# Optimization experiments

Measured on AMD Instinct MI355X. Metric: run time of the kernel, lower is better.

The kernel has to match this reference:

```python
import jax, jax.numpy as jnp
import numpy as np

# static config (matches init_kwargs)
T_K = 3      # Time_kernel
K = 3        # spatial_kernel_side_length
C = 64       # dim_hidden
H = 4        # num_head
D = 16       # dim_head
NL = 2       # num_layers
F = 3        # dim_feature
N, S1, S2 = 32, 32, 32
P = K // 2
L1 = T_K // 2
M = T_K * K * K
EPS = 1e-5


def _neighbor_mask():
    # spatial_neighbor_mask with an all-ones city mask: offset (k1,k2) is a valid
    # neighbor of cell (s1,s2) iff it lands inside the grid.
    m = np.zeros((S1, S2, K, K), dtype=bool)
    s1 = np.arange(S1); s2 = np.arange(S2)
    for k1 in range(K):
        v1 = (s1 + k1 - P >= 0) & (s1 + k1 - P < S1)
        for k2 in range(K):
            v2 = (s2 + k2 - P >= 0) & (s2 + k2 - P < S2)
            m[:, :, k1, k2] = v1[:, None] & v2[None, :]
    mf = m.reshape(S1, S2, K * K)
    # tiled across Time_kernel, flattened in (t, k1, k2) order like the torch code
    return np.tile(mf[:, :, None, :], (1, 1, T_K, 1)).reshape(S1, S2, M)

_MASK = jnp.asarray(_neighbor_mask())


def _forward(x, W_in, b_in, W_out, b_out, Wq, bq, Wk, bk, Wv, bv):
    # BatchNorm2d (training-mode batch stats, affine = identity init)
    mean = x.mean(axis=(0, 1, 2))
    var = ((x - mean) ** 2).mean(axis=(0, 1, 2))
    h = (x - mean) * jax.lax.rsqrt(var + EPS)
    h = h @ W_in + b_in  # [N,S1,S2,C]

    for l in range(NL):
        res = h  # res_block_thickness = 1 -> residual every layer
        q = (h @ Wq[l] + bq[l]).reshape(N, S1, S2, H, D)
        # spatial unfold (nn.Unfold, padding=K//2, stride=1)
        hp = jnp.pad(h, ((0, 0), (P, P), (P, P), (0, 0)))
        u = jnp.stack([jnp.stack([hp[:, k1:k1 + S1, k2:k2 + S2, :]
                                  for k2 in range(K)]) for k1 in range(K)])  # [K,K,N,S1,S2,C]
        # time unfold (zero-padded shifts along N)
        up = jnp.pad(u, ((0, 0), (0, 0), (L1, L1), (0, 0), (0, 0), (0, 0)))
        ut = jnp.stack([up[:, :, t:t + N] for t in range(T_K)])  # [T,K,K,N,S1,S2,C]
        # per-offset single-Linear MLPs (kernel_neurons=[C,C]), batched over T,K,K
        ks = jnp.einsum('tijnabc,tijcd->nabtijd', ut, Wk[l]) + bk[l]
        vs = jnp.einsum('tijnabc,tijcd->nabtijd', ut, Wv[l]) + bv[l]
        kM = ks.reshape(N, S1, S2, M, H, D)
        vM = vs.reshape(N, S1, S2, M, H, D)
        # unscaled dot-product attention over valid neighbors (masked == dropped)
        sc = jnp.einsum('nabmhd,nabhd->nabhm', kM, q)
        sc = jnp.where(_MASK[None, :, :, None, :], sc, -1e30)
        w = jax.nn.softmax(sc, axis=-1)
        h = jnp.einsum('nabhm,nabmhd->nabhd', w, vM).reshape(N, S1, S2, C)
        h = h + res

    return h @ W_out + b_out  # [N,S1,S2,F]


def setup_inputs() -> dict:
    key = jax.random.key(0)
    k = jax.random.split(key, 11)
    s = 0.05
    return {
        'x': jax.random.normal(k[0], (N, S1, S2, F), jnp.float32),
        'W_in': jax.random.normal(k[1], (F, C), jnp.float32) * s,
        'b_in': jax.random.normal(k[2], (C,), jnp.float32) * s,
        'W_out': jax.random.normal(k[3], (C, F), jnp.float32) * s,
        'b_out': jax.random.normal(k[4], (F,), jnp.float32) * s,
        'Wq': jax.random.normal(k[5], (NL, C, C), jnp.float32) * s,
        'bq': jax.random.normal(k[6], (NL, C), jnp.float32) * s,
        'Wk': jax.random.normal(k[7], (NL, T_K, K, K, C, C), jnp.float32) * s,
        'bk': jax.random.normal(k[8], (NL, T_K, K, K, C), jnp.float32) * s,
        'Wv': jax.random.normal(k[9], (NL, T_K, K, K, C, C), jnp.float32) * s,
        'bv': jax.random.normal(k[10], (NL, T_K, K, K, C), jnp.float32) * s,
    }


def reference(x, W_in, b_in, W_out, b_out, Wq, bq, Wk, bk, Wv, bv):
    return _forward(x, W_in, b_in, W_out, b_out, Wq, bq, Wk, bk, Wv, bv)
```

## Files before the change

kernel.cpp:

```cpp
#include <hip/hip_runtime.h>
#include <hip/hip_bf16.h>


typedef short short8_t __attribute__((ext_vector_type(8)));
typedef float floatx4 __attribute__((ext_vector_type(4)));

__device__ __forceinline__ short f2bs(float f) {
    __hip_bfloat16 h = __float2bfloat16(f);
    return *reinterpret_cast<short*>(&h);
}
__device__ __forceinline__ float bs2f(short s) {
    union { unsigned u; float f; } v;
    v.u = ((unsigned)(unsigned short)s) << 16;
    return v.f;
}
__device__ __forceinline__ int hn_idx(int rowid, int chunk) {
    return rowid * 64 + ((chunk ^ (rowid & 7)) << 3);
}

__global__ void prep_kernel(const float* __restrict__ Wq, const float* __restrict__ Wk,
                            const float* __restrict__ Wv, short* __restrict__ dst,
                            const float* __restrict__ x, float* __restrict__ sums) {
    if (blockIdx.x < 220) {
        int t = blockIdx.x * 256 + threadIdx.x;
        if (t >= 110 * 512) return;
        int mat  = t >> 9;
        int rem  = t & 511;
        int kk   = rem >> 8;
        int nt   = (rem >> 6) & 3;
        int lane = rem & 63;
        int krow = kk * 32 + (lane >> 4) * 8;
        int col  = nt * 16 + (lane & 15);
        const float* W;
        if (mat < 2)       W = Wq + mat * 4096;
        else if (mat < 56) W = Wk + (mat - 2) * 4096;
        else               W = Wv + (mat - 56) * 4096;
        short8_t v;
        #pragma unroll
        for (int j = 0; j < 8; ++j) v[j] = f2bs(W[(krow + j) * 64 + col]);
        *(short8_t*)&dst[(size_t)mat * 4096 + ((kk * 4 + nt) * 64 + lane) * 8] = v;
    } else {
        int bid = blockIdx.x - 220;
        int t = bid * 256 + threadIdx.x;
        const float4* x4 = (const float4*)x;
        float4 v0 = x4[t * 3 + 0], v1 = x4[t * 3 + 1], v2 = x4[t * 3 + 2];
        float vv[6];
        vv[0] = v0.x + v0.w + v1.z + v2.y;
        vv[1] = v0.y + v1.x + v1.w + v2.z;
        vv[2] = v0.z + v1.y + v2.x + v2.w;
        vv[3] = v0.x*v0.x + v0.w*v0.w + v1.z*v1.z + v2.y*v2.y;
        vv[4] = v0.y*v0.y + v1.x*v1.x + v1.w*v1.w + v2.z*v2.z;
        vv[5] = v0.z*v0.z + v1.y*v1.y + v2.x*v2.x + v2.w*v2.w;
        #pragma unroll
        for (int i = 0; i < 6; ++i) {
            #pragma unroll
            for (int off = 1; off < 64; off <<= 1) vv[i] += __shfl_xor(vv[i], off);
        }
        __shared__ float part[4][6];
        if ((threadIdx.x & 63) == 0) {
            #pragma unroll
            for (int i = 0; i < 6; ++i) part[threadIdx.x >> 6][i] = vv[i];
        }
        __syncthreads();
        if (threadIdx.x < 6)
            sums[bid * 8 + threadIdx.x] = part[0][threadIdx.x] + part[1][threadIdx.x] +
                                          part[2][threadIdx.x] + part[3][threadIdx.x];
    }
}

template <bool FIRST>
__global__ __launch_bounds__(512, 4)
void layer_fused(const float* __restrict__ x, const float* __restrict__ sums,
                 const float* __restrict__ W_in, const float* __restrict__ b_in,
                 const short* __restrict__ hbf_in, short* __restrict__ hbf_out,
                 const float* __restrict__ Wout, const float* __restrict__ bout,
                 float* __restrict__ out,
                 const short* __restrict__ wqB, const float* __restrict__ bq,
                 const short* __restrict__ wkB, const float* __restrict__ bk,
                 const short* __restrict__ wvB, const float* __restrict__ bv) {
    __shared__ short HnS[324 * 64];
    __shared__ float Waux[256];
    __shared__ float bn6[6];

    const int tid = threadIdx.x;
    const int bb0 = blockIdx.x * 4, a = blockIdx.y, nb = blockIdx.z;

    if (FIRST) {
        if (tid < 3) {
            float s = 0.f, qq = 0.f;
            #pragma unroll
            for (int p = 0; p < 32; ++p) { s += sums[p * 8 + tid]; qq += sums[p * 8 + 3 + tid]; }
            float mean = s * (1.f / 32768.f);
            float var  = qq * (1.f / 32768.f) - mean * mean;
            bn6[tid]     = mean;
            bn6[3 + tid] = rsqrtf(var + 1e-5f);
        }
        if (tid < 192)      Waux[tid] = W_in[tid];
        else if (tid < 256) Waux[tid] = b_in[tid - 192];
    } else {
        if (tid < 192)      Waux[tid] = Wout[tid];
        else if (tid < 195) Waux[tid] = bout[tid - 192];
    }
    __syncthreads();

    float mean0 = 0, mean1 = 0, mean2 = 0, rs0 = 0, rs1 = 0, rs2 = 0;
    if (FIRST) {
        mean0 = bn6[0]; mean1 = bn6[1]; mean2 = bn6[2];
        rs0 = bn6[3]; rs1 = bn6[4]; rs2 = bn6[5];
    }

    for (int id = tid; id < 2592; id += 512) {
        int rowid = id >> 3, cc = id & 7;
        int r = rowid % 18;
        int rw = rowid / 18;
        int spa = rw / 6, jcol = rw - spa * 6;
        int aa = a + spa - 1, bb = bb0 + jcol - 1;
        int n  = nb * 16 + r - 1;
        short8_t v = {0, 0, 0, 0, 0, 0, 0, 0};
        if ((unsigned)n < 32u && (unsigned)aa < 32u && (unsigned)bb < 32u) {
            int cell = (n * 32 + aa) * 32 + bb;
            if (FIRST) {
                float xn0 = (x[cell*3+0] - mean0) * rs0;
                float xn1 = (x[cell*3+1] - mean1) * rs1;
                float xn2 = (x[cell*3+2] - mean2) * rs2;
                #pragma unroll
                for (int j = 0; j < 8; ++j) {
                    int c = cc * 8 + j;
                    float h = Waux[192+c] + xn0*Waux[c] + xn1*Waux[64+c] + xn2*Waux[128+c];
                    v[j] = f2bs(h);
                }
            } else {
                v = *(const short8_t*)&hbf_in[cell * 64 + cc * 8];
            }
        }
        *(short8_t*)&HnS[hn_idx(rowid, cc)] = v;
    }
    __syncthreads();

    const int lane = tid & 63;
    const int wv8  = tid >> 6;
    const int w    = wv8 & 3;
    const int g2   = wv8 >> 2;
    const int e    = lane & 15;
    const int q    = lane >> 4;
    const int c0   = w * 16 + q * 4;

    bool va[3], vb[6];
    #pragma unroll
    for (int d = 0; d < 3; ++d) va[d] = (unsigned)(a + d - 1) < 32u;
    #pragma unroll
    for (int j = 0; j < 6; ++j) vb[j] = (unsigned)(bb0 + j - 1) < 32u;

    floatx4 qv[4];
    {
        short8_t wq0 = *(const short8_t*)&wqB[((0 * 4 + w) * 64 + lane) * 8];
        short8_t wq1 = *(const short8_t*)&wqB[((1 * 4 + w) * 64 + lane) * 8];
        const float4 bq4 = *(const float4*)&bq[c0];
        #pragma unroll
        for (int ci = 0; ci < 4; ++ci) {
            const int row = (6 + ci + 1) * 18 + e + 1;
            short8_t h0 = *(const short8_t*)&HnS[hn_idx(row, q)];
            short8_t h1 = *(const short8_t*)&HnS[hn_idx(row, 4 + q)];
            floatx4 acc = {0, 0, 0, 0};
            acc = __builtin_amdgcn_mfma_f32_16x16x32_bf16(wq0, h0, acc, 0, 0, 0);
            acc = __builtin_amdgcn_mfma_f32_16x16x32_bf16(wq1, h1, acc, 0, 0, 0);
            qv[ci][0] = acc[0] + bq4.x; qv[ci][1] = acc[1] + bq4.y;
            qv[ci][2] = acc[2] + bq4.z; qv[ci][3] = acc[3] + bq4.w;
        }
    }

    floatx4 o[4] = {{0,0,0,0},{0,0,0,0},{0,0,0,0},{0,0,0,0}};
    float ss[4] = {0.f, 0.f, 0.f, 0.f};

    const int mstart = g2 ? 14 : 0;
    const int mend   = g2 ? 27 : 14;
    for (int m = mstart; m < mend; ++m) {
        const int t  = (m * 57) >> 9;
        const int sp = m - 9 * t;
        const int di = (sp * 11) >> 5;
        const int dj = sp - 3 * di;
        if (!va[di]) continue;
        short8_t wk0 = *(const short8_t*)&wkB[m * 4096 + ((0 * 4 + w) * 64 + lane) * 8];
        short8_t wk1 = *(const short8_t*)&wkB[m * 4096 + ((1 * 4 + w) * 64 + lane) * 8];
        short8_t wv0 = *(const short8_t*)&wvB[m * 4096 + ((0 * 4 + w) * 64 + lane) * 8];
        short8_t wv1 = *(const short8_t*)&wvB[m * 4096 + ((1 * 4 + w) * 64 + lane) * 8];
        const float4 bk4 = *(const float4*)&bk[m * 64 + c0];
        const float4 bv4 = *(const float4*)&bv[m * 64 + c0];
        const int rowb = (di * 6 + dj) * 18 + e + t;
        #pragma unroll
        for (int ci = 0; ci < 4; ++ci) {
            if (!vb[dj + ci]) continue;
            const int row = rowb + ci * 18;
            short8_t h0 = *(const short8_t*)&HnS[hn_idx(row, q)];
            short8_t h1 = *(const short8_t*)&HnS[hn_idx(row, 4 + q)];
            floatx4 kacc = {0, 0, 0, 0};
            kacc = __builtin_amdgcn_mfma_f32_16x16x32_bf16(wk0, h0, kacc, 0, 0, 0);
            kacc = __builtin_amdgcn_mfma_f32_16x16x32_bf16(wk1, h1, kacc, 0, 0, 0);
            floatx4 vacc = {0, 0, 0, 0};
            vacc = __builtin_amdgcn_mfma_f32_16x16x32_bf16(wv0, h0, vacc, 0, 0, 0);
            vacc = __builtin_amdgcn_mfma_f32_16x16x32_bf16(wv1, h1, vacc, 0, 0, 0);
            float p = (kacc[0] + bk4.x) * qv[ci][0] + (kacc[1] + bk4.y) * qv[ci][1]
                    + (kacc[2] + bk4.z) * qv[ci][2] + (kacc[3] + bk4.w) * qv[ci][3];
            p += __shfl_xor(p, 16);
            p += __shfl_xor(p, 32);
            float wgt = __expf(p);
            ss[ci] += wgt;
            o[ci][0] += wgt * (vacc[0] + bv4.x);
            o[ci][1] += wgt * (vacc[1] + bv4.y);
            o[ci][2] += wgt * (vacc[2] + bv4.z);
            o[ci][3] += wgt * (vacc[3] + bv4.w);
        }
    }

    __syncthreads();
    float* stbuf = (float*)HnS;
    if (g2 == 1) {
        #pragma unroll
        for (int ci = 0; ci < 4; ++ci) {
            float* d = &stbuf[(((w * 64 + lane) * 4) + ci) * 5];
            d[0] = ss[ci];
            d[1] = o[ci][0]; d[2] = o[ci][1]; d[3] = o[ci][2]; d[4] = o[ci][3];
        }
    }
    __syncthreads();
    if (g2 == 0) {
        #pragma unroll
        for (int ci = 0; ci < 4; ++ci) {
            const float* d = &stbuf[(((w * 64 + lane) * 4) + ci) * 5];
            float inv = 1.0f / (ss[ci] + d[0]);
            o[ci][0] = (o[ci][0] + d[1]) * inv;
            o[ci][1] = (o[ci][1] + d[2]) * inv;
            o[ci][2] = (o[ci][2] + d[3]) * inv;
            o[ci][3] = (o[ci][3] + d[4]) * inv;
        }
    }

    const int n = nb * 16 + e;
    if (FIRST) {
        if (g2 == 0) {
            #pragma unroll
            for (int ci = 0; ci < 4; ++ci) {
                int cell = (n * 32 + a) * 32 + bb0 + ci;
                float xn0 = (x[cell*3+0] - mean0) * rs0;
                float xn1 = (x[cell*3+1] - mean1) * rs1;
                float xn2 = (x[cell*3+2] - mean2) * rs2;
                short4 hb; short* hbp = (short*)&hb;
                #pragma unroll
                for (int i = 0; i < 4; ++i) {
                    int c = c0 + i;
                    float res = Waux[192+c] + xn0*Waux[c] + xn1*Waux[64+c] + xn2*Waux[128+c];
                    hbp[i] = f2bs(o[ci][i] + res);
                }
                *(short4*)&hbf_out[cell * 64 + c0] = hb;
            }
        }
    } else {
        __syncthreads();
        float* hf = (float*)HnS;
        if (g2 == 0) {
            #pragma unroll
            for (int ci = 0; ci < 4; ++ci) {
                int cell = (n * 32 + a) * 32 + bb0 + ci;
                short4 hb = *(const short4*)&hbf_in[cell * 64 + c0];
                float* d = &hf[(ci * 16 + e) * 68 + c0];
                d[0] = o[ci][0] + bs2f(hb.x);
                d[1] = o[ci][1] + bs2f(hb.y);
                d[2] = o[ci][2] + bs2f(hb.z);
                d[3] = o[ci][3] + bs2f(hb.w);
            }
        }
        __syncthreads();
        if (tid < 192) {
            int rowglob = tid / 3, f = tid - rowglob * 3;
            int ci = rowglob >> 4, row = rowglob & 15;
            float acc = Waux[192 + f];
            #pragma unroll 8
            for (int cc = 0; cc < 64; ++cc) acc += hf[rowglob * 68 + cc] * Waux[cc * 3 + f];
            int nn = nb * 16 + row;
            out[((nn * 32 + a) * 32 + bb0 + ci) * 3 + f] = acc;
        }
    }
}

extern "C" void kernel_launch(void* const* d_in, const int* in_sizes, int n_in,
                              void* d_out, int out_size, void* d_ws, size_t ws_size,
                              hipStream_t stream) {
    const float* x     = (const float*)d_in[0];
    const float* W_in  = (const float*)d_in[1];
    const float* b_in  = (const float*)d_in[2];
    const float* W_out = (const float*)d_in[3];
    const float* b_out = (const float*)d_in[4];
    const float* Wq    = (const float*)d_in[5];
    const float* bq    = (const float*)d_in[6];
    const float* Wk    = (const float*)d_in[7];
    const float* bk    = (const float*)d_in[8];
    const float* Wv    = (const float*)d_in[9];
    const float* bv    = (const float*)d_in[10];

    float* ws    = (float*)d_ws;
    float* sums  = ws;
    short* h1bf  = (short*)(ws + 256);
    short* wB    = h1bf + 2097152;
    float* out   = (float*)d_out;

    prep_kernel<<<252, 256, 0, stream>>>(Wq, Wk, Wv, wB, x, sums);

    const short* wq0 = wB;                const short* wq1 = wB + 4096;
    const short* wk0 = wB + 2 * 4096;     const short* wk1 = wB + (2 + 27) * 4096;
    const short* wv0 = wB + 56 * 4096;    const short* wv1 = wB + (56 + 27) * 4096;

    dim3 grid(8, 32, 2);
    layer_fused<true><<<grid, 512, 0, stream>>>(
        x, sums, W_in, b_in, nullptr, h1bf, nullptr, nullptr, nullptr,
        wq0, bq, wk0, bk, wv0, bv);
    layer_fused<false><<<grid, 512, 0, stream>>>(
        nullptr, nullptr, nullptr, nullptr, h1bf, nullptr, W_out, b_out, out,
        wq1, bq + 64, wk1, bk + 1728, wv1, bv + 1728);
}
```

Baseline: 144.9 us.

## Switch attention projections to 32x32x16 MFMA with all-32-batch tiles

Replaces the 16x16x32 bf16 MFMA tiles with 32x32x16 tiles. Each block now covers all 32 batch (time) rows for 2 columns instead of 16 rows for 4 columns, and the weight repack in the prep kernel is changed to match the new fragment layout. Each wave computes half the channels (32) for one cell column, so two heads' logits reduce with a single cross-lane shuffle. This is meant to raise MFMA efficiency and cut duplicated shared-memory halo loads along the time axis. In exchange it uses a larger LDS tile and more accumulator registers, which may lower occupancy, and the grid becomes 16x32.

```diff
diff --git a/kernel.cpp b/kernel.cpp
--- a/kernel.cpp
+++ b/kernel.cpp
@@ -3,7 +3,7 @@
 
 
 typedef short short8_t __attribute__((ext_vector_type(8)));
-typedef float floatx4 __attribute__((ext_vector_type(4)));
+typedef float floatx16 __attribute__((ext_vector_type(16)));
 
 __device__ __forceinline__ short f2bs(float f) {
     __hip_bfloat16 h = __float2bfloat16(f);
@@ -16,6 +16,18 @@
 }
 __device__ __forceinline__ int hn_idx(int rowid, int chunk) {
     return rowid * 64 + ((chunk ^ (rowid & 7)) << 3);
+}
+__device__ __forceinline__ floatx16 bias_frag(const float* __restrict__ p) {
+    float4 f0 = *(const float4*)(p);
+    float4 f1 = *(const float4*)(p + 8);
+    float4 f2 = *(const float4*)(p + 16);
+    float4 f3 = *(const float4*)(p + 24);
+    floatx16 c;
+    c[0]=f0.x;  c[1]=f0.y;  c[2]=f0.z;  c[3]=f0.w;
+    c[4]=f1.x;  c[5]=f1.y;  c[6]=f1.z;  c[7]=f1.w;
+    c[8]=f2.x;  c[9]=f2.y;  c[10]=f2.z; c[11]=f2.w;
+    c[12]=f3.x; c[13]=f3.y; c[14]=f3.z; c[15]=f3.w;
+    return c;
 }
 
 __global__ void prep_kernel(const float* __restrict__ Wq, const float* __restrict__ Wk,
@@ -26,11 +38,11 @@
         if (t >= 110 * 512) return;
         int mat  = t >> 9;
         int rem  = t & 511;
-        int kk   = rem >> 8;
-        int nt   = (rem >> 6) & 3;
+        int kk   = rem >> 7;
+        int ch   = (rem >> 6) & 1;
         int lane = rem & 63;
-        int krow = kk * 32 + (lane >> 4) * 8;
-        int col  = nt * 16 + (lane & 15);
+        int krow = kk * 16 + (lane >> 5) * 8;
+        int col  = ch * 32 + (lane & 31);
         const float* W;
         if (mat < 2)       W = Wq + mat * 4096;
         else if (mat < 56) W = Wk + (mat - 2) * 4096;
@@ -38,7 +50,7 @@
         short8_t v;
         #pragma unroll
         for (int j = 0; j < 8; ++j) v[j] = f2bs(W[(krow + j) * 64 + col]);
-        *(short8_t*)&dst[(size_t)mat * 4096 + ((kk * 4 + nt) * 64 + lane) * 8] = v;
+        *(short8_t*)&dst[(size_t)mat * 4096 + ((kk * 2 + ch) * 64 + lane) * 8] = v;
     } else {
         int bid = blockIdx.x - 220;
         int t = bid * 256 + threadIdx.x;
@@ -78,12 +90,13 @@
                  const short* __restrict__ wqB, const float* __restrict__ bq,
                  const short* __restrict__ wkB, const float* __restrict__ bk,
                  const short* __restrict__ wvB, const float* __restrict__ bv) {
-    __shared__ short HnS[324 * 64];
+    __shared__ short HnS[408 * 64];
     __shared__ float Waux[256];
     __shared__ float bn6[6];
 
     const int tid = threadIdx.x;
-    const int bb0 = blockIdx.x * 4, a = blockIdx.y, nb = blockIdx.z;
+    const int b0  = blockIdx.x * 2;
+    const int a   = blockIdx.y;
 
     if (FIRST) {
         if (tid < 3) {
@@ -109,13 +122,13 @@
         rs0 = bn6[3]; rs1 = bn6[4]; rs2 = bn6[5];
     }
 
-    for (int id = tid; id < 2592; id += 512) {
+    for (int id = tid; id < 3264; id += 512) {
         int rowid = id >> 3, cc = id & 7;
-        int r = rowid % 18;
-        int rw = rowid / 18;
-        int spa = rw / 6, jcol = rw - spa * 6;
-        int aa = a + spa - 1, bb = bb0 + jcol - 1;
-        int n  = nb * 16 + r - 1;
+        int rw = (rowid * 241) >> 13;
+        int r  = rowid - rw * 34;
+        int spa = rw >> 2, jc = rw & 3;
+        int aa = a + spa - 1, bb = b0 + jc - 1;
+        int n  = r - 1;
         short8_t v = {0, 0, 0, 0, 0, 0, 0, 0};
         if ((unsigned)n < 32u && (unsigned)aa < 32u && (unsigned)bb < 32u) {
             int cell = (n * 32 + aa) * 32 + bb;
@@ -139,38 +152,35 @@
 
     const int lane = tid & 63;
     const int wv8  = tid >> 6;
-    const int w    = wv8 & 3;
+    const int cw   = wv8 & 1;
+    const int ch   = (wv8 >> 1) & 1;
     const int g2   = wv8 >> 2;
-    const int e    = lane & 15;
-    const int q    = lane >> 4;
-    const int c0   = w * 16 + q * 4;
-
-    bool va[3], vb[6];
+    const int nn   = lane & 31;
+    const int h5   = lane >> 5;
+    const int cb4  = ch * 32 + 4 * h5;
+
+    bool va[3], vvb[3];
     #pragma unroll
-    for (int d = 0; d < 3; ++d) va[d] = (unsigned)(a + d - 1) < 32u;
+    for (int d = 0; d < 3; ++d) {
+        va[d]  = (unsigned)(a + d - 1) < 32u;
+        vvb[d] = (unsigned)(b0 + cw + d - 1) < 32u;
+    }
+
+    floatx16 qc = bias_frag(bq + cb4);
+    {
+        const int rq = (4 + cw + 1) * 34 + nn + 1;
+        #pragma unroll
+        for (int kk = 0; kk < 4; ++kk) {
+            short8_t wf = *(const short8_t*)&wqB[((kk * 2 + ch) * 64 + lane) * 8];
+            short8_t bf = *(const short8_t*)&HnS[hn_idx(rq, kk * 2 + h5)];
+            qc = __builtin_amdgcn_mfma_f32_32x32x16_bf16(wf, bf, qc, 0, 0, 0);
+        }
+    }
+
+    floatx16 o;
     #pragma unroll
-    for (int j = 0; j < 6; ++j) vb[j] = (unsigned)(bb0 + j - 1) < 32u;
-
-    floatx4 qv[4];
-    {
-        short8_t wq0 = *(const short8_t*)&wqB[((0 * 4 + w) * 64 + lane) * 8];
-        short8_t wq1 = *(const short8_t*)&wqB[((1 * 4 + w) * 64 + lane) * 8];
-        const float4 bq4 = *(const float4*)&bq[c0];
-        #pragma unroll
-        for (int ci = 0; ci < 4; ++ci) {
-            const int row = (6 + ci + 1) * 18 + e + 1;
-            short8_t h0 = *(const short8_t*)&HnS[hn_idx(row, q)];
-            short8_t h1 = *(const short8_t*)&HnS[hn_idx(row, 4 + q)];
-            floatx4 acc = {0, 0, 0, 0};
-            acc = __builtin_amdgcn_mfma_f32_16x16x32_bf16(wq0, h0, acc, 0, 0, 0);
-            acc = __builtin_amdgcn_mfma_f32_16x16x32_bf16(wq1, h1, acc, 0, 0, 0);
-            qv[ci][0] = acc[0] + bq4.x; qv[ci][1] = acc[1] + bq4.y;
-            qv[ci][2] = acc[2] + bq4.z; qv[ci][3] = acc[3] + bq4.w;
-        }
-    }
-
-    floatx4 o[4] = {{0,0,0,0},{0,0,0,0},{0,0,0,0},{0,0,0,0}};
-    float ss[4] = {0.f, 0.f, 0.f, 0.f};
+    for (int r = 0; r < 16; ++r) o[r] = 0.f;
+    float ss0 = 0.f, ss1 = 0.f;
 
     const int mstart = g2 ? 14 : 0;
     const int mend   = g2 ? 27 : 14;
@@ -179,105 +189,109 @@
         const int sp = m - 9 * t;
         const int di = (sp * 11) >> 5;
         const int dj = sp - 3 * di;
-        if (!va[di]) continue;
-        short8_t wk0 = *(const short8_t*)&wkB[m * 4096 + ((0 * 4 + w) * 64 + lane) * 8];
-        short8_t wk1 = *(const short8_t*)&wkB[m * 4096 + ((1 * 4 + w) * 64 + lane) * 8];
-        short8_t wv0 = *(const short8_t*)&wvB[m * 4096 + ((0 * 4 + w) * 64 + lane) * 8];
-        short8_t wv1 = *(const short8_t*)&wvB[m * 4096 + ((1 * 4 + w) * 64 + lane) * 8];
-        const float4 bk4 = *(const float4*)&bk[m * 64 + c0];
-        const float4 bv4 = *(const float4*)&bv[m * 64 + c0];
-        const int rowb = (di * 6 + dj) * 18 + e + t;
-        #pragma unroll
-        for (int ci = 0; ci < 4; ++ci) {
-            if (!vb[dj + ci]) continue;
-            const int row = rowb + ci * 18;
-            short8_t h0 = *(const short8_t*)&HnS[hn_idx(row, q)];
-            short8_t h1 = *(const short8_t*)&HnS[hn_idx(row, 4 + q)];
-            floatx4 kacc = {0, 0, 0, 0};
-            kacc = __builtin_amdgcn_mfma_f32_16x16x32_bf16(wk0, h0, kacc, 0, 0, 0);
-            kacc = __builtin_amdgcn_mfma_f32_16x16x32_bf16(wk1, h1, kacc, 0, 0, 0);
-            floatx4 vacc = {0, 0, 0, 0};
-            vacc = __builtin_amdgcn_mfma_f32_16x16x32_bf16(wv0, h0, vacc, 0, 0, 0);
-            vacc = __builtin_amdgcn_mfma_f32_16x16x32_bf16(wv1, h1, vacc, 0, 0, 0);
-            float p = (kacc[0] + bk4.x) * qv[ci][0] + (kacc[1] + bk4.y) * qv[ci][1]
-                    + (kacc[2] + bk4.z) * qv[ci][2] + (kacc[3] + bk4.w) * qv[ci][3];
-            p += __shfl_xor(p, 16);
-            p += __shfl_xor(p, 32);
-            float wgt = __expf(p);
-            ss[ci] += wgt;
-            o[ci][0] += wgt * (vacc[0] + bv4.x);
-            o[ci][1] += wgt * (vacc[1] + bv4.y);
-            o[ci][2] += wgt * (vacc[2] + bv4.z);
-            o[ci][3] += wgt * (vacc[3] + bv4.w);
-        }
+        if (!va[di] || !vvb[dj]) continue;
+        const int rowb = (di * 4 + cw + dj) * 34 + nn + t;
+        short8_t bfr0 = *(const short8_t*)&HnS[hn_idx(rowb, 0 * 2 + h5)];
+        short8_t bfr1 = *(const short8_t*)&HnS[hn_idx(rowb, 1 * 2 + h5)];
+        short8_t bfr2 = *(const short8_t*)&HnS[hn_idx(rowb, 2 * 2 + h5)];
+        short8_t bfr3 = *(const short8_t*)&HnS[hn_idx(rowb, 3 * 2 + h5)];
+        const short* wkp = wkB + m * 4096 + (ch * 64 + lane) * 8;
+        const short* wvp = wvB + m * 4096 + (ch * 64 + lane) * 8;
+        floatx16 kc = bias_frag(bk + m * 64 + cb4);
+        kc = __builtin_amdgcn_mfma_f32_32x32x16_bf16(*(const short8_t*)(wkp),        bfr0, kc, 0, 0, 0);
+        kc = __builtin_amdgcn_mfma_f32_32x32x16_bf16(*(const short8_t*)(wkp + 1024), bfr1, kc, 0, 0, 0);
+        kc = __builtin_amdgcn_mfma_f32_32x32x16_bf16(*(const short8_t*)(wkp + 2048), bfr2, kc, 0, 0, 0);
+        kc = __builtin_amdgcn_mfma_f32_32x32x16_bf16(*(const short8_t*)(wkp + 3072), bfr3, kc, 0, 0, 0);
+        floatx16 vc = bias_frag(bv + m * 64 + cb4);
+        vc = __builtin_amdgcn_mfma_f32_32x32x16_bf16(*(const short8_t*)(wvp),        bfr0, vc, 0, 0, 0);
+        vc = __builtin_amdgcn_mfma_f32_32x32x16_bf16(*(const short8_t*)(wvp + 1024), bfr1, vc, 0, 0, 0);
+        vc = __builtin_amdgcn_mfma_f32_32x32x16_bf16(*(const short8_t*)(wvp + 2048), bfr2, vc, 0, 0, 0);
+        vc = __builtin_amdgcn_mfma_f32_32x32x16_bf16(*(const short8_t*)(wvp + 3072), bfr3, vc, 0, 0, 0);
+        float p0 = 0.f, p1 = 0.f;
+        #pragma unroll
+        for (int r = 0; r < 8; ++r)  p0 += kc[r] * qc[r];
+        #pragma unroll
+        for (int r = 8; r < 16; ++r) p1 += kc[r] * qc[r];
+        p0 += __shfl_xor(p0, 32);
+        p1 += __shfl_xor(p1, 32);
+        float w0 = __expf(p0), w1 = __expf(p1);
+        ss0 += w0; ss1 += w1;
+        #pragma unroll
+        for (int r = 0; r < 8; ++r)  o[r] += w0 * vc[r];
+        #pragma unroll
+        for (int r = 8; r < 16; ++r) o[r] += w1 * vc[r];
     }
 
     __syncthreads();
     float* stbuf = (float*)HnS;
+    float* st = &stbuf[((cw * 2 + ch) * 64 + lane) * 18];
     if (g2 == 1) {
-        #pragma unroll
-        for (int ci = 0; ci < 4; ++ci) {
-            float* d = &stbuf[(((w * 64 + lane) * 4) + ci) * 5];
-            d[0] = ss[ci];
-            d[1] = o[ci][0]; d[2] = o[ci][1]; d[3] = o[ci][2]; d[4] = o[ci][3];
-        }
+        st[0] = ss0; st[1] = ss1;
+        #pragma unroll
+        for (int r = 0; r < 16; ++r) st[2 + r] = o[r];
     }
     __syncthreads();
     if (g2 == 0) {
-        #pragma unroll
-        for (int ci = 0; ci < 4; ++ci) {
-            const float* d = &stbuf[(((w * 64 + lane) * 4) + ci) * 5];
-            float inv = 1.0f / (ss[ci] + d[0]);
-            o[ci][0] = (o[ci][0] + d[1]) * inv;
-            o[ci][1] = (o[ci][1] + d[2]) * inv;
-            o[ci][2] = (o[ci][2] + d[3]) * inv;
-            o[ci][3] = (o[ci][3] + d[4]) * inv;
-        }
-    }
-
-    const int n = nb * 16 + e;
+        float inv0 = 1.0f / (ss0 + st[0]);
+        float inv1 = 1.0f / (ss1 + st[1]);
+        #pragma unroll
+        for (int r = 0; r < 8; ++r)  o[r] = (o[r] + st[2 + r]) * inv0;
+        #pragma unroll
+        for (int r = 8; r < 16; ++r) o[r] = (o[r] + st[2 + r]) * inv1;
+    }
+
+    const int cell = (nn * 32 + a) * 32 + b0 + cw;
     if (FIRST) {
         if (g2 == 0) {
-            #pragma unroll
-            for (int ci = 0; ci < 4; ++ci) {
-                int cell = (n * 32 + a) * 32 + bb0 + ci;
-                float xn0 = (x[cell*3+0] - mean0) * rs0;
-                float xn1 = (x[cell*3+1] - mean1) * rs1;
-                float xn2 = (x[cell*3+2] - mean2) * rs2;
+            float xn0 = (x[cell*3+0] - mean0) * rs0;
+            float xn1 = (x[cell*3+1] - mean1) * rs1;
+            float xn2 = (x[cell*3+2] - mean2) * rs2;
+            #pragma unroll
+            for (int rg = 0; rg < 4; ++rg) {
+                int base = ch * 32 + 4 * h5 + 8 * rg;
                 short4 hb; short* hbp = (short*)&hb;
                 #pragma unroll
                 for (int i = 0; i < 4; ++i) {
-                    int c = c0 + i;
+                    int c = base + i;
                     float res = Waux[192+c] + xn0*Waux[c] + xn1*Waux[64+c] + xn2*Waux[128+c];
-                    hbp[i] = f2bs(o[ci][i] + res);
+                    hbp[i] = f2bs(o[rg * 4 + i] + res);
                 }
-                *(short4*)&hbf_out[cell * 64 + c0] = hb;
+                *(short4*)&hbf_out[cell * 64 + base] = hb;
             }
         }
     } else {
+        float resv[16];
+        if (g2 == 0) {
+            #pragma unroll
+            for (int rg = 0; rg < 4; ++rg) {
+                int base = ch * 32 + 4 * h5 + 8 * rg;
+                short4 hb = *(const short4*)&hbf_in[cell * 64 + base];
+                resv[rg*4+0] = bs2f(hb.x); resv[rg*4+1] = bs2f(hb.y);
+                resv[rg*4+2] = bs2f(hb.z); resv[rg*4+3] = bs2f(hb.w);
+            }
+        }
         __syncthreads();
         float* hf = (float*)HnS;
         if (g2 == 0) {
             #pragma unroll
-            for (int ci = 0; ci < 4; ++ci) {
-                int cell = (n * 32 + a) * 32 + bb0 + ci;
-                short4 hb = *(const short4*)&hbf_in[cell * 64 + c0];
-                float* d = &hf[(ci * 16 + e) * 68 + c0];
-                d[0] = o[ci][0] + bs2f(hb.x);
-                d[1] = o[ci][1] + bs2f(hb.y);
-                d[2] = o[ci][2] + bs2f(hb.z);
-                d[3] = o[ci][3] + bs2f(hb.w);
+            for (int rg = 0; rg < 4; ++rg) {
+                int base = ch * 32 + 4 * h5 + 8 * rg;
+                float4 d;
+                d.x = o[rg*4+0] + resv[rg*4+0];
+                d.y = o[rg*4+1] + resv[rg*4+1];
+                d.z = o[rg*4+2] + resv[rg*4+2];
+                d.w = o[rg*4+3] + resv[rg*4+3];
+                *(float4*)&hf[(cw * 32 + nn) * 68 + base] = d;
             }
         }
         __syncthreads();
         if (tid < 192) {
             int rowglob = tid / 3, f = tid - rowglob * 3;
-            int ci = rowglob >> 4, row = rowglob & 15;
+            int cw2 = rowglob >> 5, n2 = rowglob & 31;
             float acc = Waux[192 + f];
             #pragma unroll 8
             for (int cc = 0; cc < 64; ++cc) acc += hf[rowglob * 68 + cc] * Waux[cc * 3 + f];
-            int nn = nb * 16 + row;
-            out[((nn * 32 + a) * 32 + bb0 + ci) * 3 + f] = acc;
+            out[((n2 * 32 + a) * 32 + b0 + cw2) * 3 + f] = acc;
         }
     }
 }
@@ -309,7 +323,7 @@
     const short* wk0 = wB + 2 * 4096;     const short* wk1 = wB + (2 + 27) * 4096;
     const short* wv0 = wB + 56 * 4096;    const short* wv1 = wB + (56 + 27) * 4096;
 
-    dim3 grid(8, 32, 2);
+    dim3 grid(16, 32);
     layer_fused<true><<<grid, 512, 0, stream>>>(
         x, sums, W_in, b_in, nullptr, h1bf, nullptr, nullptr, nullptr,
         wq0, bq, wk0, bk, wv0, bv);
```

Result: no change. 145.0 us (+0.0%).
